# Kernel optimization log

Hardware: AMD Instinct MI355X
Metric: run time of the kernel (lower is better)

## Reference

```python
import jax, jax.numpy as jnp
import numpy as np

NUM_EXPERTS = 64
TOP_K = 2
AUX_LOSS_COEF = 0.01
HIDDEN = 2048
BATCH, SEQ = 4, 4096


def setup_inputs() -> dict:
    key = jax.random.key(0)
    k1, k2 = jax.random.split(key)
    hidden_states = jax.random.normal(k1, (BATCH, SEQ, HIDDEN), dtype=jnp.float32)
    # nn.Linear(hidden, num_experts, bias=False) weight: [E, H]
    gate_w = jax.random.normal(k2, (NUM_EXPERTS, HIDDEN), dtype=jnp.float32) / np.sqrt(HIDDEN)
    return {"hidden_states": hidden_states, "gate_w": gate_w}


def reference(hidden_states, gate_w):
    B, S, H = hidden_states.shape
    E, K = NUM_EXPERTS, TOP_K
    # gate: [B,S,H] x [E,H]^T -> [B,S,E]
    router_logits = jnp.einsum('bsh,eh->bse', hidden_states, gate_w)
    router_probs = jax.nn.softmax(router_logits, axis=-1)
    top_k_probs, expert_indices = jax.lax.top_k(router_probs, K)  # [B,S,K]
    top_k_probs = top_k_probs / jnp.sum(top_k_probs, axis=-1, keepdims=True)
    # aux load-balancing loss
    expert_mask = jax.nn.one_hot(expert_indices, E, dtype=router_probs.dtype).sum(axis=-2)  # [B,S,E]
    tokens_per_expert = expert_mask.sum(axis=(0, 1))          # [E]
    prob_per_expert = router_probs.mean(axis=(0, 1))          # [E]
    num_tokens = B * S
    aux_loss = E * jnp.sum(tokens_per_expert * prob_per_expert) / num_tokens
    router_loss = aux_loss * AUX_LOSS_COEF
    return top_k_probs, expert_indices, router_loss
```

## Files before the change

### kernel.cpp

```cpp
#include <hip/hip_runtime.h>
#include <math.h>

#define TOKENS 16384
#define HID    2048
#define NCH    16
#define TPB    128

typedef float f4 __attribute__((ext_vector_type(4)));
typedef short s8v __attribute__((ext_vector_type(8)));

#define WS_W2   262144
#define WS_PART 524288

__device__ __forceinline__ unsigned short bf16rne(float x) {
  unsigned u = __float_as_uint(x);
  return (unsigned short)((u + 0x7FFFu + ((u >> 16) & 1u)) >> 16);
}

__device__ __forceinline__ void gl16(const void* g, const void* l) {
  __builtin_amdgcn_global_load_lds(
      (const __attribute__((address_space(1))) void*)g,
      (__attribute__((address_space(3))) void*)l, 16, 0, 0);
}

#define BARK(N) { asm volatile("s_waitcnt vmcnt(" #N ") lgkmcnt(0)" ::: "memory"); \
  __builtin_amdgcn_sched_barrier(0); __builtin_amdgcn_s_barrier(); \
  __builtin_amdgcn_sched_barrier(0); }

__global__ __launch_bounds__(256) void k_pack(const float* __restrict__ gw,
                                              unsigned short* __restrict__ w1,
                                              unsigned short* __restrict__ w2) {
  int gid = blockIdx.x * 256 + threadIdx.x;
  int m = gid * 8;
  f4 a = *(const f4*)(gw + m);
  f4 b = *(const f4*)(gw + m + 4);
  float av[8] = {a.x, a.y, a.z, a.w, b.x, b.y, b.z, b.w};
  unsigned short p1[8], p2[8];
  #pragma unroll
  for (int i = 0; i < 8; ++i) {
    unsigned short h = bf16rne(av[i]);
    p1[i] = h;
    float r = av[i] - __uint_as_float((unsigned)h << 16);
    p2[i] = bf16rne(r);
  }
  *(s8v*)(w1 + m) = *(s8v*)p1;
  *(s8v*)(w2 + m) = *(s8v*)p2;
}

__global__ __launch_bounds__(512, 1) void k_main(const float* __restrict__ hid,
                                                 const unsigned short* __restrict__ w1,
                                                 const unsigned short* __restrict__ w2,
                                                 float* __restrict__ part) {
  __shared__ __align__(16) char lds[147456];
  const int tid = threadIdx.x, wave = tid >> 6, lane = tid & 63;
  const int l15 = lane & 15, ks = lane >> 4;
  const int tg = blockIdx.x >> 1, kq = blockIdx.x & 1;
  const int tok0 = tg * TPB;

  const char* hb = (const char*)hid;
  size_t asrc[4]; int adst[4];
  #pragma unroll
  for (int j = 0; j < 4; ++j) {
    int u = j * 512 + tid;
    int row = u >> 4, g = u & 15;
    asrc[j] = (size_t)(tok0 + row) * 8192 + (size_t)kq * 4096
            + (size_t)((g ^ (row & 3)) << 4);
    adst[j] = u * 16;
  }
  const char* wpb = (tid < 256) ? (const char*)w1 : (const char*)w2;
  const int bdst0 = (tid < 256) ? 32768 : 40960;
  const int tt = tid & 255;
  size_t bsrc[2]; int bdst[2];
  #pragma unroll
  for (int j = 0; j < 2; ++j) {
    int v = j * 256 + tt;
    int e = v >> 3, g = v & 7;
    bsrc[j] = (size_t)e * 4096 + (size_t)kq * 2048 + (size_t)((g ^ (e & 3)) << 4);
    bdst[j] = bdst0 + v * 16;
  }

  f4 acc[4] = {{0.f,0.f,0.f,0.f},{0.f,0.f,0.f,0.f},{0.f,0.f,0.f,0.f},{0.f,0.f,0.f,0.f}};
  const int arow = wave * 16 + l15, asw = arow & 3;

  auto stage = [&](int c, int bufb) {
    #pragma unroll
    for (int j = 0; j < 4; ++j)
      gl16(hb + asrc[j] + (size_t)c * 256, lds + bufb + adst[j]);
    #pragma unroll
    for (int j = 0; j < 2; ++j)
      gl16(wpb + bsrc[j] + (size_t)c * 128, lds + bufb + bdst[j]);
  };

  auto compute = [&](int bufb) {
    #pragma unroll
    for (int s = 0; s < 2; ++s) {
      int g0 = (s * 8 + ks * 2) ^ asw;
      int g1 = (s * 8 + ks * 2 + 1) ^ asw;
      f4 a0 = *(const f4*)(lds + bufb + arow * 256 + g0 * 16);
      f4 a1 = *(const f4*)(lds + bufb + arow * 256 + g1 * 16);
      float av[8] = {a0.x, a0.y, a0.z, a0.w, a1.x, a1.y, a1.z, a1.w};
      unsigned short p1[8], p2[8];
      #pragma unroll
      for (int i = 0; i < 8; ++i) {
        unsigned short h = bf16rne(av[i]);
        p1[i] = h;
        float r = av[i] - __uint_as_float((unsigned)h << 16);
        p2[i] = bf16rne(r);
      }
      s8v af1 = *(s8v*)p1;
      s8v af2 = *(s8v*)p2;
      #pragma unroll
      for (int nj = 0; nj < 4; ++nj) {
        int e = nj * 16 + l15;
        int g = (s * 4 + ks) ^ (e & 3);
        s8v bw1 = *(const s8v*)(lds + bufb + 32768 + e * 128 + g * 16);
        s8v bw2 = *(const s8v*)(lds + bufb + 40960 + e * 128 + g * 16);
        acc[nj] = __builtin_amdgcn_mfma_f32_16x16x32_bf16(af1, bw1, acc[nj], 0, 0, 0);
        acc[nj] = __builtin_amdgcn_mfma_f32_16x16x32_bf16(af1, bw2, acc[nj], 0, 0, 0);
        acc[nj] = __builtin_amdgcn_mfma_f32_16x16x32_bf16(af2, bw1, acc[nj], 0, 0, 0);
      }
    }
  };

  stage(0, 0);
  stage(1, 49152);
  BARK(6);

  for (int c = 0; c < NCH; ++c) {
    const int bufb = (c % 3) * 49152;
    if (c + 2 < NCH) {
      stage(c + 2, ((c + 2) % 3) * 49152);
      compute(bufb);
      BARK(6);
    } else if (c + 1 < NCH) {
      compute(bufb);
      BARK(0);
    } else {
      compute(bufb);
    }
  }

  #pragma unroll
  for (int nj = 0; nj < 4; ++nj) {
    int e = nj * 16 + l15;
    #pragma unroll
    for (int r = 0; r < 4; ++r) {
      int tl = wave * 16 + ks * 4 + r;
      part[((size_t)kq * TOKENS + (size_t)(tok0 + tl)) * 64 + e] = acc[nj][r];
    }
  }
}

__global__ __launch_bounds__(64) void k_finish(const float* __restrict__ part,
                                               float* __restrict__ out,
                                               float* __restrict__ bp) {
  __shared__ float pr[64][65];
  __shared__ float cnt[64];
  const int lane = threadIdx.x;
  const int t = blockIdx.x * 64 + lane;

  cnt[lane] = 0.f;

  float lg[64];
  const float* p0 = part + (size_t)t * 64;
  const float* p1 = part + (size_t)TOKENS * 64 + (size_t)t * 64;
  #pragma unroll
  for (int e = 0; e < 64; e += 4) {
    f4 a = *(const f4*)(p0 + e);
    f4 b = *(const f4*)(p1 + e);
    lg[e]     = a.x + b.x;
    lg[e + 1] = a.y + b.y;
    lg[e + 2] = a.z + b.z;
    lg[e + 3] = a.w + b.w;
  }

  float m = lg[0];
  #pragma unroll
  for (int e = 1; e < 64; ++e) m = fmaxf(m, lg[e]);
  float s = 0.f;
  #pragma unroll
  for (int e = 0; e < 64; ++e) { lg[e] = __expf(lg[e] - m); s += lg[e]; }
  const float inv = 1.f / s;

  float b0 = -1.f, b1 = -1.f;
  int i0 = 0, i1 = 0;
  #pragma unroll
  for (int e = 0; e < 64; ++e) {
    float p = lg[e];
    if (p > b0)      { b1 = b0; i1 = i0; b0 = p; i0 = e; }
    else if (p > b1) { b1 = p; i1 = e; }
  }
  const float rs = 1.f / (b0 + b1);
  out[(size_t)t * 2]                  = b0 * rs;
  out[(size_t)t * 2 + 1]              = b1 * rs;
  out[(size_t)TOKENS * 2 + t * 2]     = (float)i0;
  out[(size_t)TOKENS * 2 + t * 2 + 1] = (float)i1;

  #pragma unroll
  for (int e = 0; e < 64; ++e) pr[lane][e] = lg[e] * inv;
  atomicAdd(&cnt[i0], 1.f);
  atomicAdd(&cnt[i1], 1.f);
  __syncthreads();

  float sp = 0.f;
  #pragma unroll 8
  for (int tt = 0; tt < 64; ++tt) sp += pr[tt][lane];
  bp[(size_t)blockIdx.x * 128 + lane]      = sp;
  bp[(size_t)blockIdx.x * 128 + 64 + lane] = cnt[lane];
}

__global__ __launch_bounds__(1024) void k_loss(const float* __restrict__ bp,
                                               float* __restrict__ out) {
  __shared__ float partial[8][128];
  const int tid = threadIdx.x;
  const int col = tid & 127, grp = tid >> 7;
  float s = 0.f;
  #pragma unroll 4
  for (int j = 0; j < 32; ++j)
    s += bp[(size_t)(grp + j * 8) * 128 + col];
  partial[grp][col] = s;
  __syncthreads();
  if (tid < 128) {
    float t = 0.f;
    #pragma unroll
    for (int g = 0; g < 8; ++g) t += partial[g][tid];
    partial[0][tid] = t;
  }
  __syncthreads();
  if (tid < 64) {
    float v = partial[0][tid] * partial[0][64 + tid];
    #pragma unroll
    for (int d = 1; d < 64; d <<= 1) v += __shfl_xor(v, d);
    if (tid == 0)
      out[(size_t)TOKENS * 4] = 0.01f * 64.f * v / (16384.f * 16384.f);
  }
}

extern "C" void kernel_launch(void* const* d_in, const int* in_sizes, int n_in,
                              void* d_out, int out_size, void* d_ws, size_t ws_size,
                              hipStream_t stream) {
  (void)in_sizes; (void)n_in; (void)out_size; (void)ws_size;
  const float* hid = (const float*)d_in[0];
  const float* gw  = (const float*)d_in[1];
  float* out = (float*)d_out;
  char* ws = (char*)d_ws;
  unsigned short* w1 = (unsigned short*)ws;
  unsigned short* w2 = (unsigned short*)(ws + WS_W2);
  float* part  = (float*)(ws + WS_PART);
  float* bp    = (float*)ws;

  k_pack  <<<64, 256, 0, stream>>>(gw, w1, w2);
  k_main  <<<256, 512, 0, stream>>>(hid, w1, w2, part);
  k_finish<<<256, 64, 0, stream>>>(part, out, bp);
  k_loss  <<<1, 1024, 0, stream>>>(bp, out);
}
```

Baseline: 46.01 us.

## Split hidden dimension four ways with 256-token tiles when workspace allows

Adds a k_main4 kernel in which each block handles 256 tokens over a quarter of the hidden dimension, instead of 128 tokens over half. Each wave now computes two 16-row M tiles, so every staged weight fragment is reused across more tokens and total weight traffic drops. The cost is twice the partial-sum traffic: four partial slabs are written and then reduced in a templated k_finish. The new path is taken only when the workspace is large enough, and the old two-way path stays as a fallback.

```diff
diff --git a/kernel.cpp b/kernel.cpp
--- a/kernel.cpp
+++ b/kernel.cpp
@@ -3,8 +3,6 @@
 
 #define TOKENS 16384
 #define HID    2048
-#define NCH    16
-#define TPB    128
 
 typedef float f4 __attribute__((ext_vector_type(4)));
 typedef short s8v __attribute__((ext_vector_type(8)));
@@ -47,15 +45,15 @@
   *(s8v*)(w2 + m) = *(s8v*)p2;
 }
 
-__global__ __launch_bounds__(512, 1) void k_main(const float* __restrict__ hid,
-                                                 const unsigned short* __restrict__ w1,
-                                                 const unsigned short* __restrict__ w2,
-                                                 float* __restrict__ part) {
+__global__ __launch_bounds__(512, 1) void k_main2(const float* __restrict__ hid,
+                                                  const unsigned short* __restrict__ w1,
+                                                  const unsigned short* __restrict__ w2,
+                                                  float* __restrict__ part) {
   __shared__ __align__(16) char lds[147456];
   const int tid = threadIdx.x, wave = tid >> 6, lane = tid & 63;
   const int l15 = lane & 15, ks = lane >> 4;
   const int tg = blockIdx.x >> 1, kq = blockIdx.x & 1;
-  const int tok0 = tg * TPB;
+  const int tok0 = tg * 128;
 
   const char* hb = (const char*)hid;
   size_t asrc[4]; int adst[4];
@@ -90,7 +88,6 @@
     for (int j = 0; j < 2; ++j)
       gl16(wpb + bsrc[j] + (size_t)c * 128, lds + bufb + bdst[j]);
   };
-
   auto compute = [&](int bufb) {
     #pragma unroll
     for (int s = 0; s < 2; ++s) {
@@ -125,19 +122,11 @@
   stage(0, 0);
   stage(1, 49152);
   BARK(6);
-
-  for (int c = 0; c < NCH; ++c) {
+  for (int c = 0; c < 16; ++c) {
     const int bufb = (c % 3) * 49152;
-    if (c + 2 < NCH) {
-      stage(c + 2, ((c + 2) % 3) * 49152);
-      compute(bufb);
-      BARK(6);
-    } else if (c + 1 < NCH) {
-      compute(bufb);
-      BARK(0);
-    } else {
-      compute(bufb);
-    }
+    if (c + 2 < 16) { stage(c + 2, ((c + 2) % 3) * 49152); compute(bufb); BARK(6); }
+    else if (c + 1 < 16) { compute(bufb); BARK(0); }
+    else compute(bufb);
   }
 
   #pragma unroll
@@ -151,6 +140,102 @@
   }
 }
 
+__global__ __launch_bounds__(512, 1) void k_main4(const float* __restrict__ hid,
+                                                  const unsigned short* __restrict__ w1,
+                                                  const unsigned short* __restrict__ w2,
+                                                  float* __restrict__ part) {
+  __shared__ __align__(16) char lds[122880];
+  const int tid = threadIdx.x, wave = tid >> 6, lane = tid & 63;
+  const int l15 = lane & 15, ks = lane >> 4;
+  const int tg = blockIdx.x >> 2, kq = blockIdx.x & 3;
+  const int tok0 = tg * 256;
+
+  const char* hb = (const char*)hid;
+  size_t asrc[4]; int adst[4];
+  #pragma unroll
+  for (int j = 0; j < 4; ++j) {
+    int u = j * 512 + tid;
+    int row = u >> 3, g = u & 7;
+    asrc[j] = (size_t)(tok0 + row) * 8192 + (size_t)kq * 2048
+            + (size_t)((g ^ (row & 3)) << 4);
+    adst[j] = u * 16;
+  }
+  const char* wpb = (tid < 256) ? (const char*)w1 : (const char*)w2;
+  const int bdst0 = (tid < 256) ? 32768 : 36864;
+  const int tt = tid & 255;
+  const int eB = tt >> 2, gB = tt & 3;
+  const size_t bsrc = (size_t)eB * 4096 + (size_t)kq * 1024
+                    + (size_t)((gB ^ (eB & 3)) << 4);
+  const int bdst = bdst0 + tt * 16;
+
+  f4 acc[2][4];
+  #pragma unroll
+  for (int mi = 0; mi < 2; ++mi)
+    #pragma unroll
+    for (int nj = 0; nj < 4; ++nj) acc[mi][nj] = (f4){0.f, 0.f, 0.f, 0.f};
+
+  auto stage = [&](int c, int bufb) {
+    #pragma unroll
+    for (int j = 0; j < 4; ++j)
+      gl16(hb + asrc[j] + (size_t)c * 128, lds + bufb + adst[j]);
+    gl16(wpb + bsrc + (size_t)c * 64, lds + bufb + bdst);
+  };
+  auto compute = [&](int bufb) {
+    #pragma unroll
+    for (int mi = 0; mi < 2; ++mi) {
+      const int arow = wave * 32 + mi * 16 + l15, asw = arow & 3;
+      int g0 = (ks * 2) ^ asw;
+      int g1 = (ks * 2 + 1) ^ asw;
+      f4 a0 = *(const f4*)(lds + bufb + arow * 128 + g0 * 16);
+      f4 a1 = *(const f4*)(lds + bufb + arow * 128 + g1 * 16);
+      float av[8] = {a0.x, a0.y, a0.z, a0.w, a1.x, a1.y, a1.z, a1.w};
+      unsigned short p1[8], p2[8];
+      #pragma unroll
+      for (int i = 0; i < 8; ++i) {
+        unsigned short h = bf16rne(av[i]);
+        p1[i] = h;
+        float r = av[i] - __uint_as_float((unsigned)h << 16);
+        p2[i] = bf16rne(r);
+      }
+      s8v af1 = *(s8v*)p1;
+      s8v af2 = *(s8v*)p2;
+      #pragma unroll
+      for (int nj = 0; nj < 4; ++nj) {
+        int e = nj * 16 + l15;
+        int g = ks ^ (e & 3);
+        s8v bw1 = *(const s8v*)(lds + bufb + 32768 + e * 64 + g * 16);
+        s8v bw2 = *(const s8v*)(lds + bufb + 36864 + e * 64 + g * 16);
+        acc[mi][nj] = __builtin_amdgcn_mfma_f32_16x16x32_bf16(af1, bw1, acc[mi][nj], 0, 0, 0);
+        acc[mi][nj] = __builtin_amdgcn_mfma_f32_16x16x32_bf16(af1, bw2, acc[mi][nj], 0, 0, 0);
+        acc[mi][nj] = __builtin_amdgcn_mfma_f32_16x16x32_bf16(af2, bw1, acc[mi][nj], 0, 0, 0);
+      }
+    }
+  };
+
+  stage(0, 0);
+  stage(1, 40960);
+  BARK(5);
+  for (int c = 0; c < 16; ++c) {
+    const int bufb = (c % 3) * 40960;
+    if (c + 2 < 16) { stage(c + 2, ((c + 2) % 3) * 40960); compute(bufb); BARK(5); }
+    else if (c + 1 < 16) { compute(bufb); BARK(0); }
+    else compute(bufb);
+  }
+
+  #pragma unroll
+  for (int mi = 0; mi < 2; ++mi)
+    #pragma unroll
+    for (int nj = 0; nj < 4; ++nj) {
+      int e = nj * 16 + l15;
+      #pragma unroll
+      for (int r = 0; r < 4; ++r) {
+        int tl = wave * 32 + mi * 16 + ks * 4 + r;
+        part[((size_t)kq * TOKENS + (size_t)(tok0 + tl)) * 64 + e] = acc[mi][nj][r];
+      }
+    }
+}
+
+template <int NS>
 __global__ __launch_bounds__(64) void k_finish(const float* __restrict__ part,
                                                float* __restrict__ out,
                                                float* __restrict__ bp) {
@@ -162,16 +247,15 @@
   cnt[lane] = 0.f;
 
   float lg[64];
-  const float* p0 = part + (size_t)t * 64;
-  const float* p1 = part + (size_t)TOKENS * 64 + (size_t)t * 64;
   #pragma unroll
   for (int e = 0; e < 64; e += 4) {
-    f4 a = *(const f4*)(p0 + e);
-    f4 b = *(const f4*)(p1 + e);
-    lg[e]     = a.x + b.x;
-    lg[e + 1] = a.y + b.y;
-    lg[e + 2] = a.z + b.z;
-    lg[e + 3] = a.w + b.w;
+    f4 s0 = *(const f4*)(part + (size_t)t * 64 + e);
+    #pragma unroll
+    for (int q = 1; q < NS; ++q) {
+      f4 sq = *(const f4*)(part + (size_t)q * TOKENS * 64 + (size_t)t * 64 + e);
+      s0.x += sq.x; s0.y += sq.y; s0.z += sq.z; s0.w += sq.w;
+    }
+    lg[e] = s0.x; lg[e + 1] = s0.y; lg[e + 2] = s0.z; lg[e + 3] = s0.w;
   }
 
   float m = lg[0];
@@ -239,7 +323,7 @@
 extern "C" void kernel_launch(void* const* d_in, const int* in_sizes, int n_in,
                               void* d_out, int out_size, void* d_ws, size_t ws_size,
                               hipStream_t stream) {
-  (void)in_sizes; (void)n_in; (void)out_size; (void)ws_size;
+  (void)in_sizes; (void)n_in; (void)out_size;
   const float* hid = (const float*)d_in[0];
   const float* gw  = (const float*)d_in[1];
   float* out = (float*)d_out;
@@ -249,8 +333,15 @@
   float* part  = (float*)(ws + WS_PART);
   float* bp    = (float*)ws;
 
-  k_pack  <<<64, 256, 0, stream>>>(gw, w1, w2);
-  k_main  <<<256, 512, 0, stream>>>(hid, w1, w2, part);
-  k_finish<<<256, 64, 0, stream>>>(part, out, bp);
-  k_loss  <<<1, 1024, 0, stream>>>(bp, out);
-}
+  const size_t NEED4 = (size_t)WS_PART + (size_t)4 * TOKENS * 64 * 4;
+
+  k_pack<<<64, 256, 0, stream>>>(gw, w1, w2);
+  if (ws_size >= NEED4) {
+    k_main4   <<<256, 512, 0, stream>>>(hid, w1, w2, part);
+    k_finish<4><<<256, 64, 0, stream>>>(part, out, bp);
+  } else {
+    k_main2   <<<256, 512, 0, stream>>>(hid, w1, w2, part);
+    k_finish<2><<<256, 64, 0, stream>>>(part, out, bp);
+  }
+  k_loss<<<1, 1024, 0, stream>>>(bp, out);
+}
```

New measurement: 47.12 us. 1.02x slower.
